# Kernel tuning notes

Measured on AMD Instinct MI355X. Metric: run time of the kernel, lower is better.

## Reference

```python
import jax, jax.numpy as jnp
import numpy as np

N, E, B = 10000, 20000, 400
ND, ED, D = 32, 16, 64


def setup_inputs() -> dict:
    key = jax.random.key(0)
    ks = jax.random.split(key, 32)

    def lin(k, out_d, in_d):
        kw, kb = jax.random.split(k)
        s = 1.0 / np.sqrt(in_d)
        return (jax.random.uniform(kw, (out_d, in_d), jnp.float32, -s, s),
                jax.random.uniform(kb, (out_d,), jnp.float32, -s, s))

    W_in, b_in = lin(ks[0], D, ND)
    W_e1, b_e1 = lin(ks[1], D, ED)
    W_e2, b_e2 = lin(ks[2], D * D, D)
    b_conv = jax.random.uniform(ks[3], (D,), jnp.float32, -1/8.0, 1/8.0)
    W_ih, b_ih = lin(ks[4], 3 * D, D)
    W_hh, b_hh = lin(ks[5], 3 * D, D)
    W_ih_l, b_ih_l = lin(ks[6], 4 * D, 2 * D)
    W_hh_l, b_hh_l = lin(ks[7], 4 * D, D)
    W_o1, b_o1 = lin(ks[8], D, 2 * D)
    W_o2, b_o2 = lin(ks[9], 1, D)

    x = jax.random.normal(ks[10], (N, ND), jnp.float32)
    edge_attr = jax.random.normal(ks[11], (E, ED), jnp.float32)
    edge_index = jax.random.randint(ks[12], (2, E), 0, N, jnp.int64)
    batch = jnp.sort(jax.random.randint(ks[13], (N,), 0, B, jnp.int64))

    return dict(x=x, edge_attr=edge_attr,
                W_in=W_in, b_in=b_in, W_e1=W_e1, b_e1=b_e1, W_e2=W_e2, b_e2=b_e2,
                b_conv=b_conv, W_ih=W_ih, b_ih=b_ih, W_hh=W_hh, b_hh=b_hh,
                W_ih_l=W_ih_l, b_ih_l=b_ih_l, W_hh_l=W_hh_l, b_hh_l=b_hh_l,
                W_o1=W_o1, b_o1=b_o1, W_o2=W_o2, b_o2=b_o2,
                edge_index=edge_index, batch=batch)


def reference(x, edge_attr, W_in, b_in, W_e1, b_e1, W_e2, b_e2, b_conv,
              W_ih, b_ih, W_hh, b_hh, W_ih_l, b_ih_l, W_hh_l, b_hh_l,
              W_o1, b_o1, W_o2, b_o2, edge_index, batch):
    src, dst = edge_index[0], edge_index[1]

    # in_linear
    out = jax.nn.relu(x @ W_in.T + b_in)            # [N, D]
    h = out                                          # GRU hidden (layer=1, seq=1)

    # edge-conditioned weights: MLP(edge_attr) -> [E, D, D]
    ew = (jax.nn.relu(edge_attr @ W_e1.T + b_e1) @ W_e2.T + b_e2).reshape(E, D, D)
    cnt = jnp.maximum(jax.ops.segment_sum(jnp.ones((E,), x.dtype), dst, N), 1.0)

    for _ in range(3):
        # NNConv: gather src nodes, per-edge matmul, scatter-mean to dst, + bias
        msg = jnp.einsum('ed,edf->ef', out[src], ew)                 # [E, D]
        agg = jax.ops.segment_sum(msg, dst, N) / cnt[:, None] + b_conv
        m = jax.nn.relu(agg)
        # GRU cell (torch gate order r, z, n)
        gi = m @ W_ih.T + b_ih
        gh = h @ W_hh.T + b_hh
        i_r, i_z, i_n = jnp.split(gi, 3, axis=-1)
        h_r, h_z, h_n = jnp.split(gh, 3, axis=-1)
        r = jax.nn.sigmoid(i_r + h_r)
        z = jax.nn.sigmoid(i_z + h_z)
        n = jnp.tanh(i_n + r * h_n)
        h = (1.0 - z) * n + z * h
        out = h

    # Set2Set pooling, processing_steps=3
    q_star = jnp.zeros((B, 2 * D), x.dtype)
    hl = jnp.zeros((B, D), x.dtype)
    cl = jnp.zeros((B, D), x.dtype)
    for _ in range(3):
        g = q_star @ W_ih_l.T + b_ih_l + hl @ W_hh_l.T + b_hh_l
        gi_, gf_, gg_, go_ = jnp.split(g, 4, axis=-1)   # torch order i,f,g,o
        cl = jax.nn.sigmoid(gf_) * cl + jax.nn.sigmoid(gi_) * jnp.tanh(gg_)
        hl = jax.nn.sigmoid(go_) * jnp.tanh(cl)
        q = hl                                           # [B, D]
        e = jnp.sum(out * q[batch], axis=-1)             # [N]
        mmax = jax.ops.segment_max(e, batch, B)
        a = jnp.exp(e - mmax[batch])
        a = a / jax.ops.segment_sum(a, batch, B)[batch]
        r_ = jax.ops.segment_sum(a[:, None] * out, batch, B)  # [B, D]
        q_star = jnp.concatenate([q, r_], axis=-1)

    o = jax.nn.relu(q_star @ W_o1.T + b_o1) @ W_o2.T + b_o2
    return o.reshape(-1)
```

## Files before the change

### kernel.cpp

```cpp
#include <hip/hip_runtime.h>
#include <math.h>


#define Nn 10000
#define Ee 20000
#define Bb 400
#define KSTEPS 130
#define S2S_CHUNK 1024

typedef __attribute__((ext_vector_type(8))) short bf16x8_t;
typedef __attribute__((ext_vector_type(4))) float f32x4_t;

__device__ __forceinline__ float sigmoidf_(float x) { return 1.f / (1.f + expf(-x)); }

__device__ __forceinline__ void split8(const float* p, bf16x8_t& Ahi_, bf16x8_t& Alo_) {
    union { bf16x8_t v; unsigned u[4]; } hi, lo;
#pragma unroll
    for (int ii = 0; ii < 4; ++ii) {
        float pa = p[2 * ii], pb = p[2 * ii + 1];
        unsigned ua = __float_as_uint(pa), ub = __float_as_uint(pb);
        hi.u[ii] = (ua >> 16) | (ub & 0xFFFF0000u);
        float la = pa - __uint_as_float(ua & 0xFFFF0000u);
        float lb = pb - __uint_as_float(ub & 0xFFFF0000u);
        lo.u[ii] = (__float_as_uint(la) >> 16) | (__float_as_uint(lb) & 0xFFFF0000u);
    }
    Ahi_ = hi.v; Alo_ = lo.v;
}

__global__ __launch_bounds__(256) void k_in_linear(const float* __restrict__ x,
                                                   const float* __restrict__ Win,
                                                   const float* __restrict__ bin,
                                                   float* __restrict__ out) {
    int idx = blockIdx.x * 256 + threadIdx.x;
    if (idx >= Nn * 64) return;
    int n = idx >> 6, j = idx & 63;
    const float* xr = x + n * 32;
    const float* w = Win + j * 32;
    float acc = bin[j];
#pragma unroll
    for (int k = 0; k < 32; ++k) acc += xr[k] * w[k];
    out[idx] = fmaxf(acc, 0.f);
}

__global__ __launch_bounds__(256) void k_edge_mlp1(const float* __restrict__ ea,
                                                   const float* __restrict__ W1,
                                                   const float* __restrict__ b1,
                                                   float* __restrict__ eh) {
    int idx = blockIdx.x * 256 + threadIdx.x;
    if (idx >= Ee * 64) return;
    int e = idx >> 6, j = idx & 63;
    const float* ar = ea + e * 16;
    const float* w = W1 + j * 16;
    float acc = b1[j];
#pragma unroll
    for (int k = 0; k < 16; ++k) acc += ar[k] * w[k];
    eh[idx] = fmaxf(acc, 0.f);
}

__global__ __launch_bounds__(256) void k_make_Bfat(const float* __restrict__ W2,
                                                   const float* __restrict__ b2,
                                                   unsigned short* __restrict__ Bfat) {
    int idx = blockIdx.x * 256 + threadIdx.x;
    if (idx >= KSTEPS * 4096) return;
    int i  = idx & 7;
    int l  = (idx >> 3) & 63;
    int nq = (idx >> 9) & 3;
    int h  = (idx >> 11) & 1;
    int ks = idx >> 12;
    int kap = ks * 32 + (l >> 4) * 8 + i;
    int f = nq * 16 + (l & 15);
    float w;
    if (kap < 4096) {
        int q = kap >> 6, d = kap & 63;
        w = W2[(size_t)(d * 64 + f) * 64 + q];
    } else {
        int d = kap - 4096;
        w = b2[d * 64 + f];
    }
    unsigned u = __float_as_uint(w);
    unsigned short outv;
    if (h == 0) {
        outv = (unsigned short)(u >> 16);
    } else {
        float lo = w - __uint_as_float(u & 0xFFFF0000u);
        outv = (unsigned short)(__float_as_uint(lo) >> 16);
    }
    Bfat[idx] = outv;
}

__global__ __launch_bounds__(256) void k_make_Wg(const float* __restrict__ Wih,
                                                 const float* __restrict__ Whh,
                                                 unsigned short* __restrict__ Wg) {
    int idx = blockIdx.x * 256 + threadIdx.x;
    if (idx >= 4 * 2 * 16 * 64 * 8) return;
    int i  = idx & 7;
    int l  = (idx >> 3) & 63;
    int t  = (idx >> 9) & 15;
    int h  = (idx >> 13) & 1;
    int ks = idx >> 14;
    int k = ks * 32 + (l >> 4) * 8 + i;
    int u = t * 16 + (l & 15);
    int j = u & 63, part = u >> 6;
    float w = 0.f;
    if (part == 0) w = (k < 64) ? Wih[(size_t)j * 64 + k]          : Whh[(size_t)j * 64 + (k - 64)];
    if (part == 1) w = (k < 64) ? Wih[(size_t)(64 + j) * 64 + k]   : Whh[(size_t)(64 + j) * 64 + (k - 64)];
    if (part == 2) w = (k < 64) ? Wih[(size_t)(128 + j) * 64 + k]  : 0.f;
    if (part == 3) w = (k < 64) ? 0.f : Whh[(size_t)(128 + j) * 64 + (k - 64)];
    unsigned uu = __float_as_uint(w);
    unsigned short outv;
    if (h == 0) {
        outv = (unsigned short)(uu >> 16);
    } else {
        float lo = w - __uint_as_float(uu & 0xFFFF0000u);
        outv = (unsigned short)(__float_as_uint(lo) >> 16);
    }
    Wg[idx] = outv;
}

__global__ __launch_bounds__(256, 3) void k_msg_mfma(const float* __restrict__ out,
                                                     const float* __restrict__ eh,
                                                     const unsigned short* __restrict__ Bfat,
                                                     const int* __restrict__ ei,
                                                     float* __restrict__ agg) {
    __shared__ float ehs[128][20];
    __shared__ int srcs[128];
    __shared__ int dsts[128];
    int tid = threadIdx.x;
    int ebase = blockIdx.x * 128;
    int ksplit = blockIdx.y;

    int ks0 = ksplit * 32 + (ksplit < 2 ? ksplit : 2);
    int ks1 = ks0 + (ksplit < 2 ? 33 : 32);
    int q0 = ks0 >> 1;
    int qn = ((min(ks1, 128) - 1) >> 1) - q0 + 1;

    {
        int el = tid >> 1, seg = tid & 1;
        int eg = ebase + el;
        bool v = eg < Ee;
        if (seg == 0) {
            srcs[el] = v ? ei[eg] : 0;
            dsts[el] = v ? ei[Ee + eg] : 0;
        }
        const float* erow = eh + (size_t)eg * 64;
        for (int j = seg; j < qn; j += 2)
            ehs[el][j] = v ? erow[q0 + j] : 0.f;
    }
    __syncthreads();

    int lane = tid & 63;
    int wtile = tid >> 6;
    int m16 = lane & 15;
    int g = lane >> 4;
    int erA = wtile * 32 + m16;
    int erB = erA + 16;

    float a0[2][8], a1[2][8];
    {
        const float* rA = out + (size_t)srcs[erA] * 64;
        const float* rB = out + (size_t)srcs[erB] * 64;
        float4 v0, v1;
        v0 = *(const float4*)(rA + g * 8);      v1 = *(const float4*)(rA + g * 8 + 4);
        a0[0][0]=v0.x; a0[0][1]=v0.y; a0[0][2]=v0.z; a0[0][3]=v0.w;
        a0[0][4]=v1.x; a0[0][5]=v1.y; a0[0][6]=v1.z; a0[0][7]=v1.w;
        v0 = *(const float4*)(rA + 32 + g * 8); v1 = *(const float4*)(rA + 36 + g * 8);
        a1[0][0]=v0.x; a1[0][1]=v0.y; a1[0][2]=v0.z; a1[0][3]=v0.w;
        a1[0][4]=v1.x; a1[0][5]=v1.y; a1[0][6]=v1.z; a1[0][7]=v1.w;
        v0 = *(const float4*)(rB + g * 8);      v1 = *(const float4*)(rB + g * 8 + 4);
        a0[1][0]=v0.x; a0[1][1]=v0.y; a0[1][2]=v0.z; a0[1][3]=v0.w;
        a0[1][4]=v1.x; a0[1][5]=v1.y; a0[1][6]=v1.z; a0[1][7]=v1.w;
        v0 = *(const float4*)(rB + 32 + g * 8); v1 = *(const float4*)(rB + 36 + g * 8);
        a1[1][0]=v0.x; a1[1][1]=v0.y; a1[1][2]=v0.z; a1[1][3]=v0.w;
        a1[1][4]=v1.x; a1[1][5]=v1.y; a1[1][6]=v1.z; a1[1][7]=v1.w;
    }

    f32x4_t acc[2][4];
#pragma unroll
    for (int t = 0; t < 2; ++t)
#pragma unroll
        for (int nq = 0; nq < 4; ++nq) acc[t][nq] = (f32x4_t){0.f, 0.f, 0.f, 0.f};

    auto body = [&](int ks, const float (&Av)[2][8], float qA, float qB) {
        const unsigned short* bstep = Bfat + (size_t)ks * 4096;
        bf16x8_t bhi[4], blo[4];
#pragma unroll
        for (int nq = 0; nq < 4; ++nq) {
            bhi[nq] = *(const bf16x8_t*)(bstep + ((size_t)(nq * 64 + lane)) * 8);
            blo[nq] = *(const bf16x8_t*)(bstep + ((size_t)((4 + nq) * 64 + lane)) * 8);
        }
        float pA[8], pB[8];
#pragma unroll
        for (int i = 0; i < 8; ++i) { pA[i] = Av[0][i] * qA; pB[i] = Av[1][i] * qB; }
        bf16x8_t AhiA, AloA, AhiB, AloB;
        split8(pA, AhiA, AloA);
        split8(pB, AhiB, AloB);
#pragma unroll
        for (int nq = 0; nq < 4; ++nq) {
            acc[0][nq] = __builtin_amdgcn_mfma_f32_16x16x32_bf16(AhiA, bhi[nq], acc[0][nq], 0, 0, 0);
            acc[0][nq] = __builtin_amdgcn_mfma_f32_16x16x32_bf16(AhiA, blo[nq], acc[0][nq], 0, 0, 0);
            acc[0][nq] = __builtin_amdgcn_mfma_f32_16x16x32_bf16(AloA, bhi[nq], acc[0][nq], 0, 0, 0);
            acc[1][nq] = __builtin_amdgcn_mfma_f32_16x16x32_bf16(AhiB, bhi[nq], acc[1][nq], 0, 0, 0);
            acc[1][nq] = __builtin_amdgcn_mfma_f32_16x16x32_bf16(AhiB, blo[nq], acc[1][nq], 0, 0, 0);
            acc[1][nq] = __builtin_amdgcn_mfma_f32_16x16x32_bf16(AloB, bhi[nq], acc[1][nq], 0, 0, 0);
        }
    };

    for (int kp = ks0 & ~1; kp < ks1; kp += 2) {
        float qA = 1.f, qB = 1.f;
        if (kp < 128) {
            int qi = (kp >> 1) - q0;
            qA = ehs[erA][qi];
            qB = ehs[erB][qi];
        }
        if (kp >= ks0)    body(kp,     a0, qA, qB);
        if (kp + 1 < ks1) body(kp + 1, a1, qA, qB);
    }

#pragma unroll
    for (int t = 0; t < 2; ++t) {
#pragma unroll
        for (int r = 0; r < 4; ++r) {
            int el = wtile * 32 + t * 16 + g * 4 + r;
            int eg = ebase + el;
            if (eg >= Ee) continue;
            int dn = dsts[el];
#pragma unroll
            for (int nq = 0; nq < 4; ++nq)
                atomicAdd(&agg[(size_t)dn * 64 + nq * 16 + m16], acc[t][nq][r]);
        }
    }
}

__global__ __launch_bounds__(256) void k_gru_mfma(const float* __restrict__ agg,
                                                  const float* __restrict__ cnt,
                                                  const float* __restrict__ bconv,
                                                  const unsigned short* __restrict__ Wg,
                                                  const float* __restrict__ bih,
                                                  const float* __restrict__ bhh,
                                                  float* __restrict__ out) {
    __shared__ float ms[64][68];
    __shared__ float hs[64][68];
    int tid = threadIdx.x;
    int nbase = blockIdx.x * 64;

    {
        int nl = tid >> 2, seg = tid & 3;
        int ng = nbase + nl;
        bool v = ng < Nn;
        float c = v ? cnt[ng] : 1.f;
        c = c < 1.f ? 1.f : c;
        float rc = 1.f / c;
        const float* arow = agg + (size_t)ng * 64 + seg * 16;
        const float* hrow = out + (size_t)ng * 64 + seg * 16;
#pragma unroll
        for (int c4 = 0; c4 < 4; ++c4) {
            int col = seg * 16 + c4 * 4;
            float4 z = make_float4(0.f, 0.f, 0.f, 0.f);
            float4 av = v ? *(const float4*)(arow + c4 * 4) : z;
            float4 hv = v ? *(const float4*)(hrow + c4 * 4) : z;
            ms[nl][col + 0] = fmaxf(av.x * rc + bconv[col + 0], 0.f);
            ms[nl][col + 1] = fmaxf(av.y * rc + bconv[col + 1], 0.f);
            ms[nl][col + 2] = fmaxf(av.z * rc + bconv[col + 2], 0.f);
            ms[nl][col + 3] = fmaxf(av.w * rc + bconv[col + 3], 0.f);
            *(float4*)&hs[nl][col] = hv;
        }
    }
    __syncthreads();

    int lane = tid & 63;
    int wtile = tid >> 6;
    int m16 = lane & 15;
    int g = lane >> 4;
    int er = wtile * 16 + m16;

    f32x4_t acc[16];
#pragma unroll
    for (int t = 0; t < 16; ++t) acc[t] = (f32x4_t){0.f, 0.f, 0.f, 0.f};

#pragma unroll
    for (int ks = 0; ks < 4; ++ks) {
        const float* src = (ks < 2) ? &ms[er][ks * 32 + g * 8]
                                    : &hs[er][(ks - 2) * 32 + g * 8];
        float p[8];
#pragma unroll
        for (int ii = 0; ii < 8; ++ii) p[ii] = src[ii];
        bf16x8_t Ahi, Alo;
        split8(p, Ahi, Alo);
        const unsigned short* bstep = Wg + (size_t)ks * (2 * 16 * 512);
#pragma unroll
        for (int t = 0; t < 16; ++t) {
            bf16x8_t bhi = *(const bf16x8_t*)(bstep + ((size_t)t * 64 + lane) * 8);
            bf16x8_t blo = *(const bf16x8_t*)(bstep + ((size_t)(16 + t) * 64 + lane) * 8);
            acc[t] = __builtin_amdgcn_mfma_f32_16x16x32_bf16(Ahi, bhi, acc[t], 0, 0, 0);
            acc[t] = __builtin_amdgcn_mfma_f32_16x16x32_bf16(Ahi, blo, acc[t], 0, 0, 0);
            acc[t] = __builtin_amdgcn_mfma_f32_16x16x32_bf16(Alo, bhi, acc[t], 0, 0, 0);
        }
    }

#pragma unroll
    for (int t2 = 0; t2 < 4; ++t2) {
        int jj = t2 * 16 + m16;
        float br = bih[jj] + bhh[jj];
        float bz = bih[64 + jj] + bhh[64 + jj];
        float bin_ = bih[128 + jj];
        float bhn = bhh[128 + jj];
#pragma unroll
        for (int r = 0; r < 4; ++r) {
            int nl2 = wtile * 16 + g * 4 + r;
            int ng2 = nbase + nl2;
            if (ng2 >= Nn) continue;
            float rg = sigmoidf_(acc[t2][r] + br);
            float z  = sigmoidf_(acc[4 + t2][r] + bz);
            float nn = tanhf(acc[8 + t2][r] + bin_ + rg * (acc[12 + t2][r] + bhn));
            float hv = hs[nl2][jj];
            out[(size_t)ng2 * 64 + jj] = (1.f - z) * nn + z * hv;
        }
    }
}

__global__ __launch_bounds__(256) void k_count_deg(const int* __restrict__ ei,
                                                   float* __restrict__ cnt) {
    int e = blockIdx.x * 256 + threadIdx.x;
    if (e >= Ee) return;
    atomicAdd(&cnt[ei[Ee + e]], 1.f);
}

__global__ __launch_bounds__(256) void k_count_batch(const int* __restrict__ batch,
                                                     int* __restrict__ bcount) {
    int n = blockIdx.x * 256 + threadIdx.x;
    if (n >= Nn) return;
    atomicAdd(&bcount[batch[n]], 1);
}

__global__ __launch_bounds__(64) void k_scan_batch(const int* __restrict__ bcount,
                                                   int* __restrict__ bstart) {
    int lane = threadIdx.x;
    const int PER = (Bb + 63) / 64;
    int base = lane * PER;
    int v[PER];
    int s = 0;
#pragma unroll
    for (int i = 0; i < PER; ++i) {
        int idx = base + i;
        int c = (idx < Bb) ? bcount[idx] : 0;
        v[i] = s;
        s += c;
    }
    int inc = s;
#pragma unroll
    for (int o = 1; o < 64; o <<= 1) {
        int t = __shfl_up(inc, o, 64);
        if (lane >= o) inc += t;
    }
    int excl = inc - s;
    int total = __shfl(inc, 63, 64);
#pragma unroll
    for (int i = 0; i < PER; ++i) {
        int idx = base + i;
        if (idx < Bb) bstart[idx] = excl + v[i];
    }
    if (lane == 63) bstart[Bb] = total;
}

__device__ __forceinline__ float block_reduce_max_(float v, float* red, int tid) {
#pragma unroll
    for (int o = 32; o; o >>= 1) v = fmaxf(v, __shfl_xor(v, o, 64));
    if ((tid & 63) == 0) red[tid >> 6] = v;
    __syncthreads();
    float r = fmaxf(fmaxf(red[0], red[1]), fmaxf(red[2], red[3]));
    __syncthreads();
    return r;
}
__device__ __forceinline__ float block_reduce_sum_(float v, float* red, int tid) {
#pragma unroll
    for (int o = 32; o; o >>= 1) v += __shfl_xor(v, o, 64);
    if ((tid & 63) == 0) red[tid >> 6] = v;
    __syncthreads();
    float r = (red[0] + red[1]) + (red[2] + red[3]);
    __syncthreads();
    return r;
}

__global__ __launch_bounds__(256) void k_set2set(const float* __restrict__ out,
                                                 const int* __restrict__ bstart,
                                                 const float* __restrict__ Wil,
                                                 const float* __restrict__ bil,
                                                 const float* __restrict__ Whl,
                                                 const float* __restrict__ bhl,
                                                 const float* __restrict__ Wo1,
                                                 const float* __restrict__ bo1,
                                                 const float* __restrict__ Wo2,
                                                 const float* __restrict__ bo2,
                                                 float* __restrict__ outp) {
    __shared__ float qs[128];
    __shared__ float hs2[64];
    __shared__ float cs[64];
    __shared__ float g_lds[256];
    __shared__ float e_lds[S2S_CHUNK];
    __shared__ float red[4];
    __shared__ float rpart[4][64];

    int b = blockIdx.x, tid = threadIdx.x;
    int lane = tid & 63, wv = tid >> 6;
    int s = bstart[b], eend = bstart[b + 1];
    int cntb = eend - s;

    if (tid < 128) qs[tid] = 0.f;
    if (tid < 64) { hs2[tid] = 0.f; cs[tid] = 0.f; }
    __syncthreads();

    for (int step = 0; step < 3; ++step) {
        {
            int u = tid;
            float acc = bil[u] + bhl[u];
            const float4* wi = (const float4*)(Wil + (size_t)u * 128);
#pragma unroll
            for (int k4 = 0; k4 < 32; ++k4) {
                float4 w = wi[k4];
                acc += qs[k4 * 4 + 0] * w.x + qs[k4 * 4 + 1] * w.y +
                       qs[k4 * 4 + 2] * w.z + qs[k4 * 4 + 3] * w.w;
            }
            const float4* wh = (const float4*)(Whl + (size_t)u * 64);
#pragma unroll
            for (int k4 = 0; k4 < 16; ++k4) {
                float4 w = wh[k4];
                acc += hs2[k4 * 4 + 0] * w.x + hs2[k4 * 4 + 1] * w.y +
                       hs2[k4 * 4 + 2] * w.z + hs2[k4 * 4 + 3] * w.w;
            }
            g_lds[u] = acc;
        }
        __syncthreads();
        if (tid < 64) {
            float c = sigmoidf_(g_lds[64 + tid]) * cs[tid] +
                      sigmoidf_(g_lds[tid]) * tanhf(g_lds[128 + tid]);
            cs[tid] = c;
            float h = sigmoidf_(g_lds[192 + tid]) * tanhf(c);
            hs2[tid] = h;
            qs[tid] = h;
        }
        __syncthreads();

        float gmax = -INFINITY, gsum = 0.f, racc = 0.f;
        for (int c0 = s; c0 < eend; c0 += S2S_CHUNK) {
            int clen = min(S2S_CHUNK, eend - c0);
            for (int i = tid; i < clen; i += 256) {
                const float4* orow = (const float4*)(out + (size_t)(c0 + i) * 64);
                float a0 = 0.f, a1 = 0.f, a2 = 0.f, a3 = 0.f;
#pragma unroll
                for (int k4 = 0; k4 < 16; k4 += 4) {
                    float4 o0 = orow[k4], o1 = orow[k4 + 1], o2 = orow[k4 + 2], o3 = orow[k4 + 3];
                    a0 += o0.x * qs[k4 * 4 + 0]  + o0.y * qs[k4 * 4 + 1]  + o0.z * qs[k4 * 4 + 2]  + o0.w * qs[k4 * 4 + 3];
                    a1 += o1.x * qs[k4 * 4 + 4]  + o1.y * qs[k4 * 4 + 5]  + o1.z * qs[k4 * 4 + 6]  + o1.w * qs[k4 * 4 + 7];
                    a2 += o2.x * qs[k4 * 4 + 8]  + o2.y * qs[k4 * 4 + 9]  + o2.z * qs[k4 * 4 + 10] + o2.w * qs[k4 * 4 + 11];
                    a3 += o3.x * qs[k4 * 4 + 12] + o3.y * qs[k4 * 4 + 13] + o3.z * qs[k4 * 4 + 14] + o3.w * qs[k4 * 4 + 15];
                }
                e_lds[i] = (a0 + a1) + (a2 + a3);
            }
            __syncthreads();
            float m = -INFINITY;
            for (int i = tid; i < clen; i += 256) m = fmaxf(m, e_lds[i]);
            float cmax = block_reduce_max_(m, red, tid);
            float nm = fmaxf(gmax, cmax);
            float scale = expf(gmax - nm);
            gsum *= scale; racc *= scale;
            float lsum = 0.f;
            for (int i = tid; i < clen; i += 256) {
                float av = expf(e_lds[i] - nm);
                e_lds[i] = av;
                lsum += av;
            }
            gsum += block_reduce_sum_(lsum, red, tid);
            for (int i = wv; i < clen; i += 4)
                racc += e_lds[i] * out[(size_t)(c0 + i) * 64 + lane];
            gmax = nm;
            __syncthreads();
        }
        rpart[wv][lane] = racc;
        __syncthreads();
        if (tid < 64) {
            float r = (rpart[0][tid] + rpart[1][tid]) + (rpart[2][tid] + rpart[3][tid]);
            qs[64 + tid] = (cntb > 0) ? r / gsum : 0.f;
        }
        __syncthreads();
    }

    if (tid < 64) {
        float acc = bo1[tid];
        const float4* w = (const float4*)(Wo1 + (size_t)tid * 128);
#pragma unroll
        for (int k4 = 0; k4 < 32; ++k4) {
            float4 wv4 = w[k4];
            acc += qs[k4 * 4 + 0] * wv4.x + qs[k4 * 4 + 1] * wv4.y +
                   qs[k4 * 4 + 2] * wv4.z + qs[k4 * 4 + 3] * wv4.w;
        }
        acc = fmaxf(acc, 0.f);
        float t = acc * Wo2[tid];
#pragma unroll
        for (int o = 32; o; o >>= 1) t += __shfl_xor(t, o, 64);
        if (tid == 0) outp[b] = t + bo2[0];
    }
}

extern "C" void kernel_launch(void* const* d_in, const int* in_sizes, int n_in,
                              void* d_out, int out_size, void* d_ws, size_t ws_size,
                              hipStream_t stream) {
    const float* x        = (const float*)d_in[0];
    const float* ea       = (const float*)d_in[1];
    const float* W_in     = (const float*)d_in[2];
    const float* b_in     = (const float*)d_in[3];
    const float* W_e1     = (const float*)d_in[4];
    const float* b_e1     = (const float*)d_in[5];
    const float* W_e2     = (const float*)d_in[6];
    const float* b_e2     = (const float*)d_in[7];
    const float* b_conv   = (const float*)d_in[8];
    const float* W_ih     = (const float*)d_in[9];
    const float* b_ih     = (const float*)d_in[10];
    const float* W_hh     = (const float*)d_in[11];
    const float* b_hh     = (const float*)d_in[12];
    const float* W_ih_l   = (const float*)d_in[13];
    const float* b_ih_l   = (const float*)d_in[14];
    const float* W_hh_l   = (const float*)d_in[15];
    const float* b_hh_l   = (const float*)d_in[16];
    const float* W_o1     = (const float*)d_in[17];
    const float* b_o1     = (const float*)d_in[18];
    const float* W_o2     = (const float*)d_in[19];
    const float* b_o2     = (const float*)d_in[20];
    const int*   ei       = (const int*)d_in[21];
    const int*   batch    = (const int*)d_in[22];
    float* outp = (float*)d_out;

    char* base = (char*)d_ws;
    size_t off = 0;
    auto carve = [&](size_t bytes) -> void* {
        void* p = base + off;
        off = (off + bytes + 255) & ~(size_t)255;
        return p;
    };
    float* out    = (float*)carve((size_t)Nn * 64 * 4);
    float* agg    = (float*)carve((size_t)Nn * 64 * 4);
    float* eh     = (float*)carve((size_t)Ee * 64 * 4);
    unsigned short* Bfat = (unsigned short*)carve((size_t)KSTEPS * 4096 * 2);
    unsigned short* Wg   = (unsigned short*)carve((size_t)4 * 2 * 16 * 64 * 8 * 2);
    float* cnt    = (float*)carve((size_t)Nn * 4);
    int*   bcount = (int*)carve((size_t)Bb * 4);
    int*   bstart = (int*)carve((size_t)(Bb + 1) * 4);
    if (off > ws_size) return;

    hipMemsetAsync(cnt, 0, (size_t)Nn * 4, stream);
    hipMemsetAsync(bcount, 0, (size_t)Bb * 4, stream);

    k_in_linear<<<(Nn * 64) / 256, 256, 0, stream>>>(x, W_in, b_in, out);
    k_edge_mlp1<<<(Ee * 64) / 256, 256, 0, stream>>>(ea, W_e1, b_e1, eh);
    k_make_Bfat<<<(KSTEPS * 4096) / 256, 256, 0, stream>>>(W_e2, b_e2, Bfat);
    k_make_Wg<<<(4 * 2 * 16 * 64 * 8) / 256, 256, 0, stream>>>(W_ih, W_hh, Wg);
    k_count_deg<<<(Ee + 255) / 256, 256, 0, stream>>>(ei, cnt);
    k_count_batch<<<(Nn + 255) / 256, 256, 0, stream>>>(batch, bcount);
    k_scan_batch<<<1, 64, 0, stream>>>(bcount, bstart);

    int eblocks = (Ee + 127) / 128;
    int nblocks = (Nn + 63) / 64;
    for (int it = 0; it < 3; ++it) {
        hipMemsetAsync(agg, 0, (size_t)Nn * 64 * 4, stream);
        k_msg_mfma<<<dim3(eblocks, 4), 256, 0, stream>>>(out, eh, Bfat, ei, agg);
        k_gru_mfma<<<nblocks, 256, 0, stream>>>(agg, cnt, b_conv, Wg, b_ih, b_hh, out);
    }

    k_set2set<<<Bb, 256, 0, stream>>>(out, bstart, W_ih_l, b_ih_l, W_hh_l, b_hh_l,
                                      W_o1, b_o1, W_o2, b_o2, outp);
}
```

Before: 332.9 us.

## Replace atomic scatter with CSR-sorted edges and deterministic gather reduction

Edges are counting-sorted by destination into CSR order, with edge MLP outputs and source indices written in sorted positions. The message kernel now writes per-split partial messages to a buffer instead of atomically adding into agg, and the GRU kernel sums each node's contiguous message rows across splits. This removes the per-iteration agg memset and the float atomics. In exchange it adds a sort prologue, a larger message buffer that is written and then read back, and a serial per-node loop in the GRU load phase that is unbalanced across nodes.

```diff
diff --git a/kernel.cpp b/kernel.cpp
--- a/kernel.cpp
+++ b/kernel.cpp
@@ -45,6 +45,7 @@
 __global__ __launch_bounds__(256) void k_edge_mlp1(const float* __restrict__ ea,
                                                    const float* __restrict__ W1,
                                                    const float* __restrict__ b1,
+                                                   const int* __restrict__ epos,
                                                    float* __restrict__ eh) {
     int idx = blockIdx.x * 256 + threadIdx.x;
     if (idx >= Ee * 64) return;
@@ -54,7 +55,7 @@
     float acc = b1[j];
 #pragma unroll
     for (int k = 0; k < 16; ++k) acc += ar[k] * w[k];
-    eh[idx] = fmaxf(acc, 0.f);
+    eh[(size_t)epos[e] * 64 + j] = fmaxf(acc, 0.f);
 }
 
 __global__ __launch_bounds__(256) void k_make_Bfat(const float* __restrict__ W2,
@@ -117,20 +118,71 @@
     Wg[idx] = outv;
 }
 
+__global__ __launch_bounds__(256) void k_count_deg(const int* __restrict__ ei,
+                                                   int* __restrict__ deg) {
+    int e = blockIdx.x * 256 + threadIdx.x;
+    if (e >= Ee) return;
+    atomicAdd(&deg[ei[Ee + e]], 1);
+}
+
+__global__ __launch_bounds__(256) void k_scan_nodes(const int* __restrict__ deg,
+                                                    int* __restrict__ rowptr,
+                                                    int* __restrict__ wptr) {
+    __shared__ int part[256];
+    int t = threadIdx.x;
+    const int PER = (Nn + 255) / 256;
+    int b0 = t * PER;
+    int s = 0;
+    for (int i = 0; i < PER; ++i) {
+        int idx = b0 + i;
+        if (idx < Nn) s += deg[idx];
+    }
+    part[t] = s;
+    __syncthreads();
+    for (int o = 1; o < 256; o <<= 1) {
+        int u = (t >= o) ? part[t - o] : 0;
+        __syncthreads();
+        part[t] += u;
+        __syncthreads();
+    }
+    int run = part[t] - s;
+    for (int i = 0; i < PER; ++i) {
+        int idx = b0 + i;
+        if (idx < Nn) {
+            rowptr[idx] = run;
+            wptr[idx] = run;
+            run += deg[idx];
+        }
+    }
+    if (t == 255) rowptr[Nn] = run;
+}
+
+__global__ __launch_bounds__(256) void k_sort_edges(const int* __restrict__ ei,
+                                                    int* __restrict__ wptr,
+                                                    int* __restrict__ srcs,
+                                                    int* __restrict__ epos) {
+    int e = blockIdx.x * 256 + threadIdx.x;
+    if (e >= Ee) return;
+    int d = ei[Ee + e];
+    int p = atomicAdd(&wptr[d], 1);
+    srcs[p] = ei[e];
+    epos[e] = p;
+}
+
 __global__ __launch_bounds__(256, 3) void k_msg_mfma(const float* __restrict__ out,
                                                      const float* __restrict__ eh,
                                                      const unsigned short* __restrict__ Bfat,
-                                                     const int* __restrict__ ei,
-                                                     float* __restrict__ agg) {
+                                                     const int* __restrict__ srcs_g,
+                                                     float* __restrict__ msgbuf,
+                                                     int nsplit) {
     __shared__ float ehs[128][20];
     __shared__ int srcs[128];
-    __shared__ int dsts[128];
     int tid = threadIdx.x;
     int ebase = blockIdx.x * 128;
     int ksplit = blockIdx.y;
 
-    int ks0 = ksplit * 32 + (ksplit < 2 ? ksplit : 2);
-    int ks1 = ks0 + (ksplit < 2 ? 33 : 32);
+    int ks0 = (KSTEPS * ksplit) / nsplit;
+    int ks1 = (KSTEPS * (ksplit + 1)) / nsplit;
     int q0 = ks0 >> 1;
     int qn = ((min(ks1, 128) - 1) >> 1) - q0 + 1;
 
@@ -138,10 +190,7 @@
         int el = tid >> 1, seg = tid & 1;
         int eg = ebase + el;
         bool v = eg < Ee;
-        if (seg == 0) {
-            srcs[el] = v ? ei[eg] : 0;
-            dsts[el] = v ? ei[Ee + eg] : 0;
-        }
+        if (seg == 0) srcs[el] = v ? srcs_g[eg] : 0;
         const float* erow = eh + (size_t)eg * 64;
         for (int j = seg; j < qn; j += 2)
             ehs[el][j] = v ? erow[q0 + j] : 0.f;
@@ -209,8 +258,7 @@
         float qA = 1.f, qB = 1.f;
         if (kp < 128) {
             int qi = (kp >> 1) - q0;
-            qA = ehs[erA][qi];
-            qB = ehs[erB][qi];
+            if (qi >= 0) { qA = ehs[erA][qi]; qB = ehs[erB][qi]; }
         }
         if (kp >= ks0)    body(kp,     a0, qA, qB);
         if (kp + 1 < ks1) body(kp + 1, a1, qA, qB);
@@ -223,21 +271,22 @@
             int el = wtile * 32 + t * 16 + g * 4 + r;
             int eg = ebase + el;
             if (eg >= Ee) continue;
-            int dn = dsts[el];
+            float* mrow = msgbuf + ((size_t)ksplit * Ee + eg) * 64 + m16;
 #pragma unroll
             for (int nq = 0; nq < 4; ++nq)
-                atomicAdd(&agg[(size_t)dn * 64 + nq * 16 + m16], acc[t][nq][r]);
-        }
-    }
-}
-
-__global__ __launch_bounds__(256) void k_gru_mfma(const float* __restrict__ agg,
-                                                  const float* __restrict__ cnt,
+                mrow[nq * 16] = acc[t][nq][r];
+        }
+    }
+}
+
+__global__ __launch_bounds__(256) void k_gru_mfma(const float* __restrict__ msgbuf,
+                                                  const int* __restrict__ rowptr,
                                                   const float* __restrict__ bconv,
                                                   const unsigned short* __restrict__ Wg,
                                                   const float* __restrict__ bih,
                                                   const float* __restrict__ bhh,
-                                                  float* __restrict__ out) {
+                                                  float* __restrict__ out,
+                                                  int nsplit) {
     __shared__ float ms[64][68];
     __shared__ float hs[64][68];
     int tid = threadIdx.x;
@@ -247,21 +296,37 @@
         int nl = tid >> 2, seg = tid & 3;
         int ng = nbase + nl;
         bool v = ng < Nn;
-        float c = v ? cnt[ng] : 1.f;
-        c = c < 1.f ? 1.f : c;
-        float rc = 1.f / c;
-        const float* arow = agg + (size_t)ng * 64 + seg * 16;
+        int p0 = v ? rowptr[ng] : 0;
+        int p1 = v ? rowptr[ng + 1] : 0;
+        int dg = p1 - p0;
+        float rc = 1.f / (float)(dg < 1 ? 1 : dg);
+        float s[16];
+#pragma unroll
+        for (int i = 0; i < 16; ++i) s[i] = 0.f;
+        for (int sp = 0; sp < nsplit; ++sp) {
+            const float* mb = msgbuf + (size_t)sp * Ee * 64;
+            for (int p = p0; p < p1; ++p) {
+                const float* mrow = mb + (size_t)p * 64 + seg * 16;
+#pragma unroll
+                for (int c4 = 0; c4 < 4; ++c4) {
+                    float4 t4 = *(const float4*)(mrow + c4 * 4);
+                    s[c4 * 4 + 0] += t4.x;
+                    s[c4 * 4 + 1] += t4.y;
+                    s[c4 * 4 + 2] += t4.z;
+                    s[c4 * 4 + 3] += t4.w;
+                }
+            }
+        }
         const float* hrow = out + (size_t)ng * 64 + seg * 16;
+        float4 z = make_float4(0.f, 0.f, 0.f, 0.f);
 #pragma unroll
         for (int c4 = 0; c4 < 4; ++c4) {
             int col = seg * 16 + c4 * 4;
-            float4 z = make_float4(0.f, 0.f, 0.f, 0.f);
-            float4 av = v ? *(const float4*)(arow + c4 * 4) : z;
             float4 hv = v ? *(const float4*)(hrow + c4 * 4) : z;
-            ms[nl][col + 0] = fmaxf(av.x * rc + bconv[col + 0], 0.f);
-            ms[nl][col + 1] = fmaxf(av.y * rc + bconv[col + 1], 0.f);
-            ms[nl][col + 2] = fmaxf(av.z * rc + bconv[col + 2], 0.f);
-            ms[nl][col + 3] = fmaxf(av.w * rc + bconv[col + 3], 0.f);
+            ms[nl][col + 0] = fmaxf(s[c4 * 4 + 0] * rc + bconv[col + 0], 0.f);
+            ms[nl][col + 1] = fmaxf(s[c4 * 4 + 1] * rc + bconv[col + 1], 0.f);
+            ms[nl][col + 2] = fmaxf(s[c4 * 4 + 2] * rc + bconv[col + 2], 0.f);
+            ms[nl][col + 3] = fmaxf(s[c4 * 4 + 3] * rc + bconv[col + 3], 0.f);
             *(float4*)&hs[nl][col] = hv;
         }
     }
@@ -316,13 +381,6 @@
             out[(size_t)ng2 * 64 + jj] = (1.f - z) * nn + z * hv;
         }
     }
-}
-
-__global__ __launch_bounds__(256) void k_count_deg(const int* __restrict__ ei,
-                                                   float* __restrict__ cnt) {
-    int e = blockIdx.x * 256 + threadIdx.x;
-    if (e >= Ee) return;
-    atomicAdd(&cnt[ei[Ee + e]], 1.f);
 }
 
 __global__ __launch_bounds__(256) void k_count_batch(const int* __restrict__ batch,
@@ -536,33 +594,48 @@
         off = (off + bytes + 255) & ~(size_t)255;
         return p;
     };
-    float* out    = (float*)carve((size_t)Nn * 64 * 4);
-    float* agg    = (float*)carve((size_t)Nn * 64 * 4);
-    float* eh     = (float*)carve((size_t)Ee * 64 * 4);
-    unsigned short* Bfat = (unsigned short*)carve((size_t)KSTEPS * 4096 * 2);
-    unsigned short* Wg   = (unsigned short*)carve((size_t)4 * 2 * 16 * 64 * 8 * 2);
-    float* cnt    = (float*)carve((size_t)Nn * 4);
-    int*   bcount = (int*)carve((size_t)Bb * 4);
-    int*   bstart = (int*)carve((size_t)(Bb + 1) * 4);
+
+    int ns = 4;
+    float *out, *msgbuf, *eh;
+    unsigned short *Bfat, *Wg;
+    int *srcs, *epos, *rowptr, *wptr, *deg, *bcount, *bstart;
+    for (;; ns >>= 1) {
+        off = 0;
+        out    = (float*)carve((size_t)Nn * 64 * 4);
+        msgbuf = (float*)carve((size_t)ns * Ee * 64 * 4);
+        eh     = (float*)carve((size_t)Ee * 64 * 4);
+        Bfat   = (unsigned short*)carve((size_t)KSTEPS * 4096 * 2);
+        Wg     = (unsigned short*)carve((size_t)4 * 2 * 16 * 64 * 8 * 2);
+        srcs   = (int*)carve((size_t)Ee * 4);
+        epos   = (int*)carve((size_t)Ee * 4);
+        rowptr = (int*)carve((size_t)(Nn + 1) * 4);
+        wptr   = (int*)carve((size_t)Nn * 4);
+        deg    = (int*)carve((size_t)Nn * 4);
+        bcount = (int*)carve((size_t)Bb * 4);
+        bstart = (int*)carve((size_t)(Bb + 1) * 4);
+        if (off <= ws_size || ns == 1) break;
+    }
     if (off > ws_size) return;
 
-    hipMemsetAsync(cnt, 0, (size_t)Nn * 4, stream);
+    hipMemsetAsync(deg, 0, (size_t)Nn * 4, stream);
     hipMemsetAsync(bcount, 0, (size_t)Bb * 4, stream);
 
+    k_count_deg<<<(Ee + 255) / 256, 256, 0, stream>>>(ei, deg);
+    k_scan_nodes<<<1, 256, 0, stream>>>(deg, rowptr, wptr);
+    k_sort_edges<<<(Ee + 255) / 256, 256, 0, stream>>>(ei, wptr, srcs, epos);
+
     k_in_linear<<<(Nn * 64) / 256, 256, 0, stream>>>(x, W_in, b_in, out);
-    k_edge_mlp1<<<(Ee * 64) / 256, 256, 0, stream>>>(ea, W_e1, b_e1, eh);
+    k_edge_mlp1<<<(Ee * 64) / 256, 256, 0, stream>>>(ea, W_e1, b_e1, epos, eh);
     k_make_Bfat<<<(KSTEPS * 4096) / 256, 256, 0, stream>>>(W_e2, b_e2, Bfat);
     k_make_Wg<<<(4 * 2 * 16 * 64 * 8) / 256, 256, 0, stream>>>(W_ih, W_hh, Wg);
-    k_count_deg<<<(Ee + 255) / 256, 256, 0, stream>>>(ei, cnt);
     k_count_batch<<<(Nn + 255) / 256, 256, 0, stream>>>(batch, bcount);
     k_scan_batch<<<1, 64, 0, stream>>>(bcount, bstart);
 
     int eblocks = (Ee + 127) / 128;
     int nblocks = (Nn + 63) / 64;
     for (int it = 0; it < 3; ++it) {
-        hipMemsetAsync(agg, 0, (size_t)Nn * 64 * 4, stream);
-        k_msg_mfma<<<dim3(eblocks, 4), 256, 0, stream>>>(out, eh, Bfat, ei, agg);
-        k_gru_mfma<<<nblocks, 256, 0, stream>>>(agg, cnt, b_conv, Wg, b_ih, b_hh, out);
+        k_msg_mfma<<<dim3(eblocks, ns), 256, 0, stream>>>(out, eh, Bfat, srcs, msgbuf, ns);
+        k_gru_mfma<<<nblocks, 256, 0, stream>>>(msgbuf, rowptr, b_conv, Wg, b_ih, b_hh, out, ns);
     }
 
     k_set2set<<<Bb, 256, 0, stream>>>(out, bstart, W_ih_l, b_ih_l, W_hh_l, b_hh_l,
```

After: 340.2 us. 1.02x slower.
